# Optimization experiments

Hardware: AMD Instinct MI355X
Metric: run time of the kernel (lower is better)

Reference implementation:

```python
import jax, jax.numpy as jnp
import numpy as np

N_NODES = 8192
N_EDGES = 262144
IN_DIM = 256
HID = 256
OUT_DIM = 64
PATH_DIM = 64
N_HEADS = 4


def setup_inputs() -> dict:
    key = jax.random.key(0)
    ks = jax.random.split(key, 16)
    s = 0.05
    x = jax.random.normal(ks[0], (N_NODES, IN_DIM), dtype=jnp.float32)
    edge_index = jax.random.randint(ks[1], (2, N_EDGES), 0, N_NODES, dtype=jnp.int32)
    return {
        "x": x,
        "edge_index": edge_index,
        # pathway encoder Linear(IN_DIM, PATH_DIM)
        "pe_w": jax.random.normal(ks[2], (IN_DIM, PATH_DIM), jnp.float32) * s,
        "pe_b": jax.random.normal(ks[3], (PATH_DIM,), jnp.float32) * s,
        # MultiheadAttention packed in-proj [3E, E] and out-proj [E, E]
        "in_proj_w": jax.random.normal(ks[4], (3 * PATH_DIM, PATH_DIM), jnp.float32) * s,
        "in_proj_b": jax.random.normal(ks[5], (3 * PATH_DIM,), jnp.float32) * s,
        "out_proj_w": jax.random.normal(ks[6], (PATH_DIM, PATH_DIM), jnp.float32) * s,
        "out_proj_b": jax.random.normal(ks[7], (PATH_DIM,), jnp.float32) * s,
        # GCN layer weights (in_dim, out_dim) + bias
        "w1": jax.random.normal(ks[8], (IN_DIM + PATH_DIM, HID), jnp.float32) * s,
        "b1": jax.random.normal(ks[9], (HID,), jnp.float32) * s,
        "w2": jax.random.normal(ks[10], (HID, HID), jnp.float32) * s,
        "b2": jax.random.normal(ks[11], (HID,), jnp.float32) * s,
        "w3": jax.random.normal(ks[12], (HID, OUT_DIM), jnp.float32) * s,
        "b3": jax.random.normal(ks[13], (OUT_DIM,), jnp.float32) * s,
    }


def mha_self(x, in_proj_w, in_proj_b, out_proj_w, out_proj_b):
    # unbatched nn.MultiheadAttention: x [N, E], Q=K=V=x
    N, E = x.shape
    dh = E // N_HEADS
    qkv = x @ in_proj_w.T + in_proj_b  # [N, 3E]
    q, k, v = jnp.split(qkv, 3, axis=-1)
    # [H, N, dh]
    q = q.reshape(N, N_HEADS, dh).transpose(1, 0, 2)
    k = k.reshape(N, N_HEADS, dh).transpose(1, 0, 2)
    v = v.reshape(N, N_HEADS, dh).transpose(1, 0, 2)
    scores = jnp.einsum('hnd,hmd->hnm', q, k) / jnp.sqrt(jnp.float32(dh))
    attn = jax.nn.softmax(scores, axis=-1)
    out = jnp.einsum('hnm,hmd->hnd', attn, v)  # [H, N, dh]
    out = out.transpose(1, 0, 2).reshape(N, E)
    return out @ out_proj_w.T + out_proj_b


def gcn_conv(h, edge_index, w, b, num_nodes):
    # PyG GCNConv: add self loops, symmetric normalization, linear, scatter-add, bias
    src = jnp.concatenate([edge_index[0], jnp.arange(num_nodes, dtype=edge_index.dtype)])
    dst = jnp.concatenate([edge_index[1], jnp.arange(num_nodes, dtype=edge_index.dtype)])
    deg = jax.ops.segment_sum(jnp.ones_like(dst, dtype=h.dtype), dst, num_segments=num_nodes)
    dinv = jnp.where(deg > 0, jax.lax.rsqrt(jnp.maximum(deg, 1e-12)), 0.0)
    hw = h @ w  # [N, out]
    norm = (dinv[src] * dinv[dst])[:, None]
    msg = hw[src] * norm
    out = jax.ops.segment_sum(msg, dst, num_segments=num_nodes)
    return out + b


def reference(x, edge_index, pe_w, pe_b, in_proj_w, in_proj_b, out_proj_w, out_proj_b,
              w1, b1, w2, b2, w3, b3):
    N = x.shape[0]
    pf = x @ pe_w + pe_b  # pathway encoder
    pa = mha_self(pf, in_proj_w, in_proj_b, out_proj_w, out_proj_b)
    h = jnp.concatenate([x, pa], axis=-1)  # [N, IN_DIM + PATH_DIM]
    h = jax.nn.relu(gcn_conv(h, edge_index, w1, b1, N))  # dropout is identity (eval)
    h = jax.nn.relu(gcn_conv(h, edge_index, w2, b2, N))
    h = gcn_conv(h, edge_index, w3, b3, N)
    return h
```

## Files before the change

kernel.cpp:

```cpp
#include <hip/hip_runtime.h>
#include <hip/hip_bf16.h>

#define N_NODES 8192
#define N_EDGES 262144
#define IN_DIM 256
#define HID 256
#define OUT_DIM 64
#define PATH_DIM 64
#define NHEADS 4
#define DH 16

typedef __attribute__((ext_vector_type(8))) short bf16x8;
typedef __attribute__((ext_vector_type(4))) float f32x4;

__device__ __forceinline__ ushort f2bf(float f) {
  union { float f; unsigned int u; } c;
  c.f = f;
  unsigned int u = c.u;
  u += 0x7fffu + ((u >> 16) & 1u);
  return (ushort)(u >> 16);
}

__device__ __forceinline__ float fast_exp2(float x) {
  float r;
  asm("v_exp_f32 %0, %1" : "=v"(r) : "v"(x));
  return r;
}

__device__ __forceinline__ unsigned pack_bf16(float a, float b) {
  union { __hip_bfloat162 h; unsigned u; } c;
  c.h = __float22bfloat162_rn(make_float2(a, b));
  return c.u;
}


__global__ __launch_bounds__(256) void init_graph(int* deg, int* cursor) {
  int i = blockIdx.x * 256 + threadIdx.x;
  if (i < N_NODES) { deg[i] = 1; cursor[i] = 0; }
}

__global__ __launch_bounds__(256) void count_deg(const int* __restrict__ dst,
                                                 int* __restrict__ deg) {
  int e = blockIdx.x * 256 + threadIdx.x;
  if (e < N_EDGES) atomicAdd(&deg[dst[e]], 1);
}

__global__ __launch_bounds__(256) void scan_rows(const int* __restrict__ deg,
                                                 int* __restrict__ row_off,
                                                 float* __restrict__ dinv) {
  __shared__ int part[256];
  int t = threadIdx.x;
  int base = t * 32;
  int local[32];
  int s = 0;
  #pragma unroll
  for (int i = 0; i < 32; ++i) {
    int c = deg[base + i] - 1;
    local[i] = s;
    s += c;
  }
  part[t] = s;
  __syncthreads();
  for (int d = 1; d < 256; d <<= 1) {
    int v = (t >= d) ? part[t - d] : 0;
    __syncthreads();
    part[t] += v;
    __syncthreads();
  }
  int prev = (t == 0) ? 0 : part[t - 1];
  #pragma unroll
  for (int i = 0; i < 32; ++i) {
    row_off[base + i] = prev + local[i];
    dinv[base + i] = rsqrtf((float)deg[base + i]);
  }
}

__global__ __launch_bounds__(256) void fill_csr(const int* __restrict__ src,
                                                const int* __restrict__ dst,
                                                const int* __restrict__ row_off,
                                                int* __restrict__ cursor,
                                                int* __restrict__ csr) {
  int e = blockIdx.x * 256 + threadIdx.x;
  if (e < N_EDGES) {
    int d = dst[e];
    int p = atomicAdd(&cursor[d], 1);
    csr[row_off[d] + p] = src[e];
  }
}


__global__ __launch_bounds__(256) void transpose_w(const float* __restrict__ W,
                                                   float* __restrict__ Wt,
                                                   int R, int C) {
  int i = blockIdx.x * 256 + threadIdx.x;
  if (i < R * C) {
    int r = i / C, c = i % C;
    Wt[c * R + r] = W[i];
  }
}

__global__ __launch_bounds__(256) void convert_qkv(const float* __restrict__ qkv,
                                                   ushort* __restrict__ Qbf,
                                                   ushort* __restrict__ Kbf,
                                                   ushort* __restrict__ Vtb) {
  const int tg = blockIdx.x * 256 + threadIdx.x;
  const int h = tg >> 13;
  const int n = tg & 8191;
  const float SC = 0.36067376022224085f;
  const float* base = qkv + (size_t)n * 192 + h * 16;
  ushort* qd = Qbf + ((size_t)h * 8192 + n) * 32;
  ushort* kd = Kbf + ((size_t)h * 8192 + n) * 32;
  ushort4 zz = make_ushort4(0, 0, 0, 0);
  #pragma unroll
  for (int i = 0; i < 16; i += 4) {
    float4 q4 = *reinterpret_cast<const float4*>(base + i);
    float4 k4 = *reinterpret_cast<const float4*>(base + 64 + i);
    float4 v4 = *reinterpret_cast<const float4*>(base + 128 + i);
    *reinterpret_cast<ushort4*>(qd + i) =
        make_ushort4(f2bf(q4.x * SC), f2bf(q4.y * SC), f2bf(q4.z * SC), f2bf(q4.w * SC));
    *reinterpret_cast<ushort4*>(kd + i) =
        make_ushort4(f2bf(k4.x), f2bf(k4.y), f2bf(k4.z), f2bf(k4.w));
    *reinterpret_cast<ushort4*>(qd + 16 + i) = zz;
    *reinterpret_cast<ushort4*>(kd + 16 + i) = zz;
    Vtb[((size_t)h * 16 + i + 0) * 8192 + n] = f2bf(v4.x);
    Vtb[((size_t)h * 16 + i + 1) * 8192 + n] = f2bf(v4.y);
    Vtb[((size_t)h * 16 + i + 2) * 8192 + n] = f2bf(v4.z);
    Vtb[((size_t)h * 16 + i + 3) * 8192 + n] = f2bf(v4.w);
  }
}


template <bool RELU, bool BIAS>
__global__ __launch_bounds__(256) void gemm_tile(const float* __restrict__ A1, int K1,
                                                 const float* __restrict__ A2, int K2,
                                                 const float* __restrict__ B,
                                                 const float* __restrict__ bias,
                                                 float* __restrict__ C, int N) {
  __shared__ __align__(16) float As[16][64];
  __shared__ __align__(16) float Bs[16][68];
  const int K = K1 + K2;
  const int bm = blockIdx.y * 64;
  const int bn = blockIdx.x * 64;
  const int t = threadIdx.x;
  const int tx = t & 15, ty = t >> 4;
  const int am = t >> 2;
  const int ak = (t & 3) << 2;
  const int bk = t >> 4;
  const int bn4 = (t & 15) << 2;
  float acc[4][4] = {};
  for (int k0 = 0; k0 < K; k0 += 16) {
    int kk = k0 + ak;
    int row = bm + am;
    float4 av;
    if (kk < K1)
      av = *reinterpret_cast<const float4*>(A1 + (size_t)row * K1 + kk);
    else
      av = *reinterpret_cast<const float4*>(A2 + (size_t)row * K2 + (kk - K1));
    As[ak + 0][am] = av.x;
    As[ak + 1][am] = av.y;
    As[ak + 2][am] = av.z;
    As[ak + 3][am] = av.w;
    float4 bv = *reinterpret_cast<const float4*>(B + (size_t)(k0 + bk) * N + bn + bn4);
    *reinterpret_cast<float4*>(&Bs[bk][bn4]) = bv;
    __syncthreads();
    #pragma unroll
    for (int k = 0; k < 16; ++k) {
      float4 a = *reinterpret_cast<const float4*>(&As[k][ty << 2]);
      float4 b = *reinterpret_cast<const float4*>(&Bs[k][tx << 2]);
      acc[0][0] += a.x * b.x; acc[0][1] += a.x * b.y; acc[0][2] += a.x * b.z; acc[0][3] += a.x * b.w;
      acc[1][0] += a.y * b.x; acc[1][1] += a.y * b.y; acc[1][2] += a.y * b.z; acc[1][3] += a.y * b.w;
      acc[2][0] += a.z * b.x; acc[2][1] += a.z * b.y; acc[2][2] += a.z * b.z; acc[2][3] += a.z * b.w;
      acc[3][0] += a.w * b.x; acc[3][1] += a.w * b.y; acc[3][2] += a.w * b.z; acc[3][3] += a.w * b.w;
    }
    __syncthreads();
  }
  #pragma unroll
  for (int i = 0; i < 4; ++i) {
    int row = bm + (ty << 2) + i;
    float4 o = make_float4(acc[i][0], acc[i][1], acc[i][2], acc[i][3]);
    if (BIAS) {
      float4 bv = *reinterpret_cast<const float4*>(bias + bn + (tx << 2));
      o.x += bv.x; o.y += bv.y; o.z += bv.z; o.w += bv.w;
    }
    if (RELU) {
      o.x = fmaxf(o.x, 0.f); o.y = fmaxf(o.y, 0.f);
      o.z = fmaxf(o.z, 0.f); o.w = fmaxf(o.w, 0.f);
    }
    *reinterpret_cast<float4*>(C + (size_t)row * N + bn + (tx << 2)) = o;
  }
}


__global__ __launch_bounds__(256) void attn_mfma2(const ushort* __restrict__ Qbf,
                                                  const ushort* __restrict__ Kbf,
                                                  const ushort* __restrict__ Vtb,
                                                  float* __restrict__ attn_out) {
  const int h  = blockIdx.y;
  const int qb = blockIdx.x;
  const int t  = threadIdx.x;
  const int wv = t >> 6;
  const int l  = t & 63;
  const int lg = l >> 4;
  const int lc = l & 15;

  __shared__ __align__(16) ushort Ps[2][64][64];
  __shared__ __align__(16) ushort Vls[3][16][64];
  __shared__ float wred[4][64];

  bf16x8 qf[4];
  {
    const ushort* qbase = Qbf + ((size_t)h * 8192 + qb * 64) * 32;
    #pragma unroll
    for (int qt = 0; qt < 4; ++qt)
      qf[qt] = *reinterpret_cast<const bf16x8*>(qbase + (qt * 16 + lc) * 32 + lg * 8);
  }

  const ushort* kbase = Kbf + (size_t)h * 8192 * 32 + (wv * 16 + lc) * 32 + lg * 8;

  const int vrow = t >> 4;
  const int vcol8 = t & 15;
  const ushort* vsrc = Vtb + ((size_t)h * 16 + vrow) * 8192 + vcol8 * 4;
  const int vdst = vrow * 128 + (((vcol8 >> 1) ^ (vrow & 7)) << 4) + (vcol8 & 1) * 8;

  const int pw_off = (((wv * 2 + (lg >> 1)) ^ (lc & 7)) << 4) + (lg & 1) * 8;
  int pr_off[2], vr_off[2];
  #pragma unroll
  for (int half = 0; half < 2; ++half) {
    int g = (half * 4 + lg) ^ (lc & 7);
    pr_off[half] = (wv * 16 + lc) * 128 + g * 16;
    vr_off[half] = lc * 128 + g * 16;
  }

  char* ps_base  = (char*)&Ps[0][0][0];
  char* vls_base = (char*)&Vls[0][0][0];

  *reinterpret_cast<ushort4*>(vls_base + vdst) =
      *reinterpret_cast<const ushort4*>(vsrc);

  f32x4 oacc = {0.f, 0.f, 0.f, 0.f};
  float wsumP[4] = {0.f, 0.f, 0.f, 0.f};

  __syncthreads();

  for (int c = 0; c < 128; ++c) {
    const int mc = c * 64;
    ushort4 vpre;
    const bool dopre = (c + 1 < 128);
    if (dopre) vpre = *reinterpret_cast<const ushort4*>(vsrc + mc + 64);

    bf16x8 kf = *reinterpret_cast<const bf16x8*>(kbase + (size_t)mc * 32);

    f32x4 s[4];
    #pragma unroll
    for (int qt = 0; qt < 4; ++qt) {
      f32x4 z = {0.f, 0.f, 0.f, 0.f};
      s[qt] = __builtin_amdgcn_mfma_f32_16x16x32_bf16(kf, qf[qt], z, 0, 0, 0);
    }

    char* psb = ps_base + (c & 1) * 8192;
    #pragma unroll
    for (int qt = 0; qt < 4; ++qt) {
      float e0 = fast_exp2(s[qt][0]);
      float e1 = fast_exp2(s[qt][1]);
      float e2 = fast_exp2(s[qt][2]);
      float e3 = fast_exp2(s[qt][3]);
      wsumP[qt] += (e0 + e1) + (e2 + e3);
      uint2 pk;
      pk.x = pack_bf16(e0, e1);
      pk.y = pack_bf16(e2, e3);
      *reinterpret_cast<uint2*>(psb + (qt * 16 + lc) * 128 + pw_off) = pk;
    }

    if (dopre)
      *reinterpret_cast<ushort4*>(vls_base + ((c + 1) % 3) * 2048 + vdst) = vpre;

    __syncthreads();

    char* vlb = vls_base + (c % 3) * 2048;
    #pragma unroll
    for (int half = 0; half < 2; ++half) {
      bf16x8 pf = *reinterpret_cast<const bf16x8*>(psb + pr_off[half]);
      bf16x8 vf = *reinterpret_cast<const bf16x8*>(vlb + vr_off[half]);
      oacc = __builtin_amdgcn_mfma_f32_16x16x32_bf16(pf, vf, oacc, 0, 0, 0);
    }
  }

  #pragma unroll
  for (int qt = 0; qt < 4; ++qt) {
    float v = wsumP[qt];
    v += __shfl_xor(v, 16);
    v += __shfl_xor(v, 32);
    wsumP[qt] = v;
  }
  if (lg == 0) {
    #pragma unroll
    for (int qt = 0; qt < 4; ++qt) wred[wv][qt * 16 + lc] = wsumP[qt];
  }
  __syncthreads();

  #pragma unroll
  for (int r = 0; r < 4; ++r) {
    const int qrow = wv * 16 + lg * 4 + r;
    float ws = wred[0][qrow] + wred[1][qrow] + wred[2][qrow] + wred[3][qrow];
    attn_out[(size_t)(qb * 64 + qrow) * 64 + h * 16 + lc] = oacc[r] / ws;
  }
}


template <int C, bool RELU>
__global__ __launch_bounds__(256) void aggregate(const float* __restrict__ hw,
                                                 const int* __restrict__ csr,
                                                 const int* __restrict__ row_off,
                                                 const int* __restrict__ deg,
                                                 const float* __restrict__ dinv,
                                                 const float* __restrict__ bias,
                                                 float* __restrict__ out) {
  const int w = threadIdx.x >> 6, l = threadIdx.x & 63;
  const int r = blockIdx.x * 4 + w;
  const float dr = dinv[r];
  const int off = row_off[r];
  const int cnt = deg[r] - 1;

  if constexpr (C == 256) {
    const int c = l << 2;
    float4 a = *reinterpret_cast<const float4*>(hw + (size_t)r * C + c);
    float ax = dr * a.x, ay = dr * a.y, az = dr * a.z, aw = dr * a.w;
    for (int e = 0; e < cnt; ++e) {
      int s = csr[off + e];
      float ws = dinv[s];
      float4 hv = *reinterpret_cast<const float4*>(hw + (size_t)s * C + c);
      ax += ws * hv.x; ay += ws * hv.y; az += ws * hv.z; aw += ws * hv.w;
    }
    float4 bv = *reinterpret_cast<const float4*>(bias + c);
    float4 o;
    o.x = dr * ax + bv.x; o.y = dr * ay + bv.y;
    o.z = dr * az + bv.z; o.w = dr * aw + bv.w;
    if (RELU) {
      o.x = fmaxf(o.x, 0.f); o.y = fmaxf(o.y, 0.f);
      o.z = fmaxf(o.z, 0.f); o.w = fmaxf(o.w, 0.f);
    }
    *reinterpret_cast<float4*>(out + (size_t)r * C + c) = o;
  } else {
    float a = dr * hw[(size_t)r * C + l];
    for (int e = 0; e < cnt; ++e) {
      int s = csr[off + e];
      a += dinv[s] * hw[(size_t)s * C + l];
    }
    float o = dr * a + bias[l];
    if (RELU) o = fmaxf(o, 0.f);
    out[(size_t)r * C + l] = o;
  }
}


extern "C" void kernel_launch(void* const* d_in, const int* in_sizes, int n_in,
                              void* d_out, int out_size, void* d_ws, size_t ws_size,
                              hipStream_t stream) {
  const float* x          = (const float*)d_in[0];
  const int*   ei         = (const int*)d_in[1];
  const float* pe_w       = (const float*)d_in[2];
  const float* pe_b       = (const float*)d_in[3];
  const float* in_proj_w  = (const float*)d_in[4];
  const float* in_proj_b  = (const float*)d_in[5];
  const float* out_proj_w = (const float*)d_in[6];
  const float* out_proj_b = (const float*)d_in[7];
  const float* w1         = (const float*)d_in[8];
  const float* b1         = (const float*)d_in[9];
  const float* w2         = (const float*)d_in[10];
  const float* b2         = (const float*)d_in[11];
  const float* w3         = (const float*)d_in[12];
  const float* b3         = (const float*)d_in[13];

  const int* esrc = ei;
  const int* edst = ei + N_EDGES;

  char* ws = (char*)d_ws;
  size_t o = 0;
  auto take = [&](size_t n) {
    char* p = ws + o;
    o += (n + 255) & ~(size_t)255;
    return p;
  };
  float* pf       = (float*)take((size_t)N_NODES * PATH_DIM * 4);
  float* qkv      = (float*)take((size_t)N_NODES * 3 * PATH_DIM * 4);
  float* attn_out = (float*)take((size_t)N_NODES * PATH_DIM * 4);
  float* pa       = (float*)take((size_t)N_NODES * PATH_DIM * 4);
  float* hw       = (float*)take((size_t)N_NODES * HID * 4);
  float* h1       = (float*)take((size_t)N_NODES * HID * 4);
  float* h2       = (float*)take((size_t)N_NODES * HID * 4);
  float* Wt_in    = (float*)take((size_t)3 * PATH_DIM * PATH_DIM * 4);
  float* Wt_out   = (float*)take((size_t)PATH_DIM * PATH_DIM * 4);
  float* dinv     = (float*)take((size_t)N_NODES * 4);
  int*   deg      = (int*)take((size_t)N_NODES * 4);
  int*   cursor   = (int*)take((size_t)N_NODES * 4);
  int*   row_off  = (int*)take((size_t)N_NODES * 4);
  int*   csr      = (int*)take((size_t)N_EDGES * 4);

  ushort* Qbf = (ushort*)h1;
  ushort* Kbf = Qbf + (size_t)NHEADS * N_NODES * 32;
  ushort* Vtb = Kbf + (size_t)NHEADS * N_NODES * 32;

  init_graph<<<N_NODES / 256, 256, 0, stream>>>(deg, cursor);
  count_deg<<<N_EDGES / 256, 256, 0, stream>>>(edst, deg);
  scan_rows<<<1, 256, 0, stream>>>(deg, row_off, dinv);
  fill_csr<<<N_EDGES / 256, 256, 0, stream>>>(esrc, edst, row_off, cursor, csr);

  transpose_w<<<(192 * 64 + 255) / 256, 256, 0, stream>>>(in_proj_w, Wt_in, 192, 64);
  transpose_w<<<(64 * 64 + 255) / 256, 256, 0, stream>>>(out_proj_w, Wt_out, 64, 64);

  gemm_tile<false, true><<<dim3(1, 128), 256, 0, stream>>>(x, IN_DIM, nullptr, 0, pe_w, pe_b, pf, PATH_DIM);
  gemm_tile<false, true><<<dim3(3, 128), 256, 0, stream>>>(pf, PATH_DIM, nullptr, 0, Wt_in, in_proj_b, qkv, 3 * PATH_DIM);

  convert_qkv<<<(N_NODES * NHEADS) / 256, 256, 0, stream>>>(qkv, Qbf, Kbf, Vtb);
  attn_mfma2<<<dim3(128, 4), 256, 0, stream>>>(Qbf, Kbf, Vtb, attn_out);

  gemm_tile<false, true><<<dim3(1, 128), 256, 0, stream>>>(attn_out, PATH_DIM, nullptr, 0, Wt_out, out_proj_b, pa, PATH_DIM);

  gemm_tile<false, false><<<dim3(4, 128), 256, 0, stream>>>(x, IN_DIM, pa, PATH_DIM, w1, nullptr, hw, HID);
  aggregate<256, true><<<N_NODES / 4, 256, 0, stream>>>(hw, csr, row_off, deg, dinv, b1, h1);
  gemm_tile<false, false><<<dim3(4, 128), 256, 0, stream>>>(h1, HID, nullptr, 0, w2, nullptr, hw, HID);
  aggregate<256, true><<<N_NODES / 4, 256, 0, stream>>>(hw, csr, row_off, deg, dinv, b2, h2);
  gemm_tile<false, false><<<dim3(1, 128), 256, 0, stream>>>(h2, HID, nullptr, 0, w3, nullptr, hw, OUT_DIM);
  aggregate<64, false><<<N_NODES / 4, 256, 0, stream>>>(hw, csr, row_off, deg, dinv, b3, (float*)d_out);
}
```

Baseline: 328.1 us.

## Split attention over the key dimension with a separate combine kernel

Splits each attention block's loop over the 8192 keys into 4 independent chunks via a third grid dimension, which raises the block count from 512 to 2048. Each block writes an unnormalized partial output and a partial softmax denominator, reusing the h2 and pa buffers as scratch. A new combine kernel sums the partials and divides. This targets low GPU occupancy and the long serial key loop in the attention kernel. In exchange it adds an extra launch and extra global traffic for the partials. It relies on the softmax not subtracting a running max, so the partial sums can simply be added.

After: 304.0 us. -7.3%, faster.

```diff
diff --git a/kernel.cpp b/kernel.cpp
--- a/kernel.cpp
+++ b/kernel.cpp
@@ -9,6 +9,7 @@
 #define PATH_DIM 64
 #define NHEADS 4
 #define DH 16
+#define KSPLIT 4
 
 typedef __attribute__((ext_vector_type(8))) short bf16x8;
 typedef __attribute__((ext_vector_type(4))) float f32x4;
@@ -191,12 +192,14 @@
 }
 
 
-__global__ __launch_bounds__(256) void attn_mfma2(const ushort* __restrict__ Qbf,
+__global__ __launch_bounds__(256) void attn_mfma3(const ushort* __restrict__ Qbf,
                                                   const ushort* __restrict__ Kbf,
                                                   const ushort* __restrict__ Vtb,
-                                                  float* __restrict__ attn_out) {
+                                                  float* __restrict__ Opart,
+                                                  float* __restrict__ Wpart) {
   const int h  = blockIdx.y;
   const int qb = blockIdx.x;
+  const int kz = blockIdx.z;
   const int t  = threadIdx.x;
   const int wv = t >> 6;
   const int l  = t & 63;
@@ -215,11 +218,12 @@
       qf[qt] = *reinterpret_cast<const bf16x8*>(qbase + (qt * 16 + lc) * 32 + lg * 8);
   }
 
-  const ushort* kbase = Kbf + (size_t)h * 8192 * 32 + (wv * 16 + lc) * 32 + lg * 8;
+  const ushort* kbase =
+      Kbf + (size_t)h * 8192 * 32 + ((size_t)kz * 2048 + wv * 16 + lc) * 32 + lg * 8;
 
   const int vrow = t >> 4;
   const int vcol8 = t & 15;
-  const ushort* vsrc = Vtb + ((size_t)h * 16 + vrow) * 8192 + vcol8 * 4;
+  const ushort* vsrc = Vtb + ((size_t)h * 16 + vrow) * 8192 + kz * 2048 + vcol8 * 4;
   const int vdst = vrow * 128 + (((vcol8 >> 1) ^ (vrow & 7)) << 4) + (vcol8 & 1) * 8;
 
   const int pw_off = (((wv * 2 + (lg >> 1)) ^ (lc & 7)) << 4) + (lg & 1) * 8;
@@ -242,10 +246,10 @@
 
   __syncthreads();
 
-  for (int c = 0; c < 128; ++c) {
+  for (int c = 0; c < 2048 / 64; ++c) {
     const int mc = c * 64;
     ushort4 vpre;
-    const bool dopre = (c + 1 < 128);
+    const bool dopre = (c + 1 < 2048 / 64);
     if (dopre) vpre = *reinterpret_cast<const ushort4*>(vsrc + mc + 64);
 
     bf16x8 kf = *reinterpret_cast<const bf16x8*>(kbase + (size_t)mc * 32);
@@ -298,12 +302,38 @@
   }
   __syncthreads();
 
+  const size_t obase = ((size_t)(kz * NHEADS + h) * N_NODES + qb * 64);
   #pragma unroll
   for (int r = 0; r < 4; ++r) {
     const int qrow = wv * 16 + lg * 4 + r;
-    float ws = wred[0][qrow] + wred[1][qrow] + wred[2][qrow] + wred[3][qrow];
-    attn_out[(size_t)(qb * 64 + qrow) * 64 + h * 16 + lc] = oacc[r] / ws;
-  }
+    Opart[(obase + qrow) * 16 + lc] = oacc[r];
+  }
+  if (t < 64) {
+    float ws = wred[0][t] + wred[1][t] + wred[2][t] + wred[3][t];
+    Wpart[obase + t] = ws;
+  }
+}
+
+__global__ __launch_bounds__(256) void attn_combine(const float* __restrict__ Opart,
+                                                    const float* __restrict__ Wpart,
+                                                    float* __restrict__ attn_out) {
+  int i = blockIdx.x * 256 + threadIdx.x;
+  int dq = i & 3;
+  int hn = i >> 2;
+  int h = hn >> 13;
+  int n = hn & 8191;
+  float4 acc = make_float4(0.f, 0.f, 0.f, 0.f);
+  float ws = 0.f;
+  #pragma unroll
+  for (int s = 0; s < KSPLIT; ++s) {
+    const size_t row = ((size_t)(s * NHEADS + h) * N_NODES + n);
+    float4 v = *reinterpret_cast<const float4*>(Opart + row * 16 + dq * 4);
+    acc.x += v.x; acc.y += v.y; acc.z += v.z; acc.w += v.w;
+    ws += Wpart[row];
+  }
+  float inv = 1.f / ws;
+  float4 o = make_float4(acc.x * inv, acc.y * inv, acc.z * inv, acc.w * inv);
+  *reinterpret_cast<float4*>(attn_out + (size_t)n * 64 + h * 16 + dq * 4) = o;
 }
 
 
@@ -399,6 +429,8 @@
   ushort* Qbf = (ushort*)h1;
   ushort* Kbf = Qbf + (size_t)NHEADS * N_NODES * 32;
   ushort* Vtb = Kbf + (size_t)NHEADS * N_NODES * 32;
+  float* Opart = h2;
+  float* Wpart = pa;
 
   init_graph<<<N_NODES / 256, 256, 0, stream>>>(deg, cursor);
   count_deg<<<N_EDGES / 256, 256, 0, stream>>>(edst, deg);
@@ -412,7 +444,8 @@
   gemm_tile<false, true><<<dim3(3, 128), 256, 0, stream>>>(pf, PATH_DIM, nullptr, 0, Wt_in, in_proj_b, qkv, 3 * PATH_DIM);
 
   convert_qkv<<<(N_NODES * NHEADS) / 256, 256, 0, stream>>>(qkv, Qbf, Kbf, Vtb);
-  attn_mfma2<<<dim3(128, 4), 256, 0, stream>>>(Qbf, Kbf, Vtb, attn_out);
+  attn_mfma3<<<dim3(128, 4, KSPLIT), 256, 0, stream>>>(Qbf, Kbf, Vtb, Opart, Wpart);
+  attn_combine<<<(NHEADS * N_NODES * 4) / 256, 256, 0, stream>>>(Opart, Wpart, attn_out);
 
   gemm_tile<false, true><<<dim3(1, 128), 256, 0, stream>>>(attn_out, PATH_DIM, nullptr, 0, Wt_out, out_proj_b, pa, PATH_DIM);
 
```
